# Performance work log

Measured on AMD Instinct MI355X. Metric: run time of the kernel, lower is better.

The kernel has to match this reference:

```python
import jax, jax.numpy as jnp
import numpy as np

B, C, H, W = 8, 512, 56, 56
CI = C // 2  # inter_channels
EPS = 1e-5   # BatchNorm eps


def setup_inputs() -> dict:
    key = jax.random.key(0)
    ks = jax.random.split(key, 11)
    s = 0.02
    return {
        "x": jax.random.normal(ks[0], (B, C, H, W), jnp.float32),
        "theta_w": jax.random.normal(ks[1], (CI, C), jnp.float32) * s,
        "theta_b": jnp.zeros((CI,), jnp.float32),
        "phi_w": jax.random.normal(ks[2], (CI, C), jnp.float32) * s,
        "phi_b": jnp.zeros((CI,), jnp.float32),
        "g_w": jax.random.normal(ks[3], (CI, C), jnp.float32) * s,
        "g_b": jnp.zeros((CI,), jnp.float32),
        "w_w": jax.random.normal(ks[4], (C, CI), jnp.float32) * s,
        "w_b": jnp.zeros((C,), jnp.float32),
        "bn_gamma": jax.random.normal(ks[5], (C,), jnp.float32) * 0.1,
        "bn_beta": jax.random.normal(ks[6], (C,), jnp.float32) * 0.1,
    }


def reference(x, theta_w, theta_b, phi_w, phi_b, g_w, g_b, w_w, w_b, bn_gamma, bn_beta):
    b, c, h, w = x.shape
    n = h * w

    def proj(wt, bi):  # 1x1 conv -> [b, out, n]
        return (jnp.einsum('bchw,oc->bohw', x, wt) + bi[None, :, None, None]).reshape(b, -1, n)

    theta_x = proj(theta_w, theta_b).transpose(0, 2, 1)  # [b, n, ci]
    phi_x = proj(phi_w, phi_b)                           # [b, ci, n]
    g_x = proj(g_w, g_b).transpose(0, 2, 1)             # [b, n, ci]

    f = jnp.einsum('bnc,bcm->bnm', theta_x, phi_x)       # [b, n, n] unscaled scores
    f_div_c = jax.nn.softmax(f, axis=-1)
    y = jnp.einsum('bnm,bmc->bnc', f_div_c, g_x)         # [b, n, ci]
    y = y.transpose(0, 2, 1).reshape(b, -1, h, w)        # [b, ci, h, w]

    w_y = jnp.einsum('bchw,oc->bohw', y, w_w) + w_b[None, :, None, None]
    # BatchNorm2d (training mode, batch statistics over B,H,W per channel)
    mean = w_y.mean(axis=(0, 2, 3))
    var = w_y.var(axis=(0, 2, 3))
    w_y = (w_y - mean[None, :, None, None]) * jax.lax.rsqrt(var[None, :, None, None] + EPS)
    w_y = w_y * bn_gamma[None, :, None, None] + bn_beta[None, :, None, None]
    return w_y + x
```

## Files before the change

### kernel.cpp

```cpp
#include <hip/hip_runtime.h>
#include <hip/hip_bf16.h>


typedef unsigned short u16;
typedef unsigned int u32;
typedef __attribute__((ext_vector_type(8))) short short8;
typedef __attribute__((ext_vector_type(4))) float floatx4;

#define B_   8
#define C_   512
#define CI_  256
#define N_   3136
#define BN_  25088

__device__ __forceinline__ u16 f2b(float f) {
    return __builtin_bit_cast(u16, __float2bfloat16(f));
}
__device__ __forceinline__ float b2f(u16 u) {
    return __bfloat162float(__builtin_bit_cast(__hip_bfloat16, u));
}
__device__ __forceinline__ floatx4 mfma16(short8 a, short8 b, floatx4 c) {
    return __builtin_amdgcn_mfma_f32_16x16x32_bf16(a, b, c, 0, 0, 0);
}
__device__ __forceinline__ void gload_lds16(const u16* g, u16* l) {
    __builtin_amdgcn_global_load_lds(
        (const __attribute__((address_space(1))) u32*)g,
        (__attribute__((address_space(3))) u32*)l, 16, 0, 0);
}

__global__ void detect_dtype(const u32* __restrict__ xw, int* __restrict__ flag)
{
    __shared__ int cnt;
    if (threadIdx.x == 0) cnt = 0;
    __syncthreads();
    int c = 0;
    for (int i = 0; i < 16; ++i) {
        u32 w = xw[threadIdx.x * 16 + i];
        u32 e = (w >> 7) & 0xFF;
        c += (e >= 118 && e <= 130) ? 1 : 0;
    }
    atomicAdd(&cnt, c);
    __syncthreads();
    if (threadIdx.x == 0) *flag = (2 * cnt > 4096) ? 1 : 0;
}

__global__ __launch_bounds__(256) void convert_params(
    const void* tw, const void* tb, const void* pw, const void* pb,
    const void* gw, const void* gbi, const void* ww, const void* wb,
    const void* gamma, const void* beta,
    u16* __restrict__ dst, const int* __restrict__ flag)
{
    const void* srcs[10] = {tw, tb, pw, pb, gw, gbi, ww, wb, gamma, beta};
    const int ns[10] = {131072, 256, 131072, 256, 131072, 256, 131072, 512, 512, 512};
    int seg = blockIdx.y;
    int off = 0;
    for (int s = 0; s < 10; ++s) { if (s == seg) break; off += ns[s]; }
    const void* src = srcs[seg];
    int n = ns[seg];
    int i0 = (blockIdx.x * 256 + threadIdx.x) * 8;
    if (i0 >= n) return;
    const int fl = *flag;
    u16* d = dst + off;
    for (int k = 0; k < 8; ++k) {
        int i = i0 + k;
        if (i < n)
            d[i] = fl ? ((const u16*)src)[i] : f2b(((const float*)src)[i]);
    }
}

__global__ __launch_bounds__(256) void transpose_x(
    const void* __restrict__ in, u16* __restrict__ out,
    const int* __restrict__ flag)
{
    __shared__ u16 tile[64][68];
    const int fl = *flag;
    const int t = threadIdx.x;
    const long base = (long)blockIdx.z * (long)C_ * (long)N_;
    const int c0 = blockIdx.x * 64, r0 = blockIdx.y * 64;
    const int lr = t >> 3;
    const int lc = (t & 7) * 8;
#pragma unroll
    for (int j = 0; j < 2; ++j) {
        int rr = lr + 32 * j;
        long eoff = base + (long)(r0 + rr) * N_ + c0 + lc;
        u16 v[8] __attribute__((aligned(16)));
        if (fl) {
            const u16* pi = (const u16*)in + eoff;
            *(uint64_t*)&v[0] = *(const uint64_t*)pi;
            *(uint64_t*)&v[4] = *(const uint64_t*)(pi + 4);
        } else {
            const float* pi = (const float*)in + eoff;
            floatx4 a = *(const floatx4*)pi;
            floatx4 b4 = *(const floatx4*)(pi + 4);
#pragma unroll
            for (int k = 0; k < 4; ++k) { v[k] = f2b(a[k]); v[4 + k] = f2b(b4[k]); }
        }
        *(uint64_t*)&tile[rr][lc] = *(const uint64_t*)&v[0];
        *(uint64_t*)&tile[rr][lc + 4] = *(const uint64_t*)&v[4];
    }
    __syncthreads();
#pragma unroll
    for (int j = 0; j < 2; ++j) {
        int oc = lr + 32 * j;
        int ob = (t & 7) * 8;
        u16 vals[8] __attribute__((aligned(16)));
#pragma unroll
        for (int k = 0; k < 8; ++k) vals[k] = tile[ob + k][oc];
        u16* po = out + (long)blockIdx.z * N_ * C_ + (long)(c0 + oc) * C_ + r0 + ob;
        *(uint64_t*)po = *(const uint64_t*)vals;
        *(uint64_t*)(po + 4) = *(const uint64_t*)(vals + 4);
    }
}

__global__ __launch_bounds__(256) void transpose64(
    const u16* __restrict__ in, u16* __restrict__ out, int R, int Cc)
{
    __shared__ u16 tile[64][68];
    const int t = threadIdx.x;
    const long base = (long)blockIdx.z * (long)R * (long)Cc;
    const int c0 = blockIdx.x * 64, r0 = blockIdx.y * 64;
    const int lr = t >> 3;
    const int lc = (t & 7) * 8;
#pragma unroll
    for (int j = 0; j < 2; ++j) {
        int rr = lr + 32 * j;
        const u16* pi = in + base + (long)(r0 + rr) * Cc + c0 + lc;
        *(uint64_t*)&tile[rr][lc] = *(const uint64_t*)pi;
        *(uint64_t*)&tile[rr][lc + 4] = *(const uint64_t*)(pi + 4);
    }
    __syncthreads();
#pragma unroll
    for (int j = 0; j < 2; ++j) {
        int oc = lr + 32 * j;
        int ob = (t & 7) * 8;
        u16 vals[8] __attribute__((aligned(16)));
#pragma unroll
        for (int k = 0; k < 8; ++k) vals[k] = tile[ob + k][oc];
        u16* po = out + base + (long)(c0 + oc) * R + r0 + ob;
        *(uint64_t*)po = *(const uint64_t*)vals;
        *(uint64_t*)(po + 4) = *(const uint64_t*)(vals + 4);
    }
}

template<int K>
__global__ __launch_bounds__(256, 3) void gemm128(
    const u16* __restrict__ A,
    const u16* __restrict__ BtBase,
    const u16* __restrict__ biasBase,
    u16* __restrict__ OutBase,
    int ncols, long bstride, long ostride)
{
    __shared__ __attribute__((aligned(16))) u16 Asf[2][8][64][8];
    __shared__ __attribute__((aligned(16))) u16 Bsf[2][8][64][8];

    const int t = threadIdx.x;
    const int wave = t >> 6, lane = t & 63;
    const int q = lane >> 4, lx = lane & 15;
    const int m0 = blockIdx.x * 128;
    const int n0 = blockIdx.y * 128;
    const u16* Bt = BtBase + (long)blockIdx.z * bstride;
    const u16* bias = biasBase + (long)blockIdx.z * bstride;
    u16* Out = OutBase + (long)blockIdx.z * ostride;

    floatx4 zero4 = {0.f, 0.f, 0.f, 0.f};
    floatx4 acc[4][4];
#pragma unroll
    for (int i = 0; i < 4; ++i)
#pragma unroll
        for (int j = 0; j < 4; ++j) acc[i][j] = zero4;

    auto stage = [&](int buf, int k0) {
#pragma unroll
        for (int i = 0; i < 2; ++i) {
            int rg = wave * 2 + i;
            gload_lds16(A + (long)(m0 + rg * 16 + lx) * K + k0 + q * 8,
                        &Asf[buf][rg][0][0]);
            gload_lds16(Bt + (long)(n0 + rg * 16 + lx) * K + k0 + q * 8,
                        &Bsf[buf][rg][0][0]);
        }
    };

    stage(0, 0);
    const int rg0 = (wave >> 1) * 4, cg0 = (wave & 1) * 4;
    const int NS = K / 32;
    for (int s = 0; s < NS; ++s) {
        const int buf = s & 1;
        __syncthreads();
        if (s + 1 < NS) stage(buf ^ 1, (s + 1) * 32);
        short8 af[4], bfr[4];
#pragma unroll
        for (int i = 0; i < 4; ++i)
            af[i] = *(const short8*)&Asf[buf][rg0 + i][lane][0];
#pragma unroll
        for (int j = 0; j < 4; ++j)
            bfr[j] = *(const short8*)&Bsf[buf][cg0 + j][lane][0];
#pragma unroll
        for (int i = 0; i < 4; ++i)
#pragma unroll
            for (int j = 0; j < 4; ++j)
                acc[i][j] = mfma16(af[i], bfr[j], acc[i][j]);
    }

    const int wr = (wave >> 1) * 64, wc = (wave & 1) * 64;
#pragma unroll
    for (int j = 0; j < 4; ++j) {
        int col = n0 + wc + j * 16 + lx;
        float bv = b2f(bias[col]);
#pragma unroll
        for (int i = 0; i < 4; ++i) {
#pragma unroll
            for (int r = 0; r < 4; ++r) {
                int row = m0 + wr + i * 16 + q * 4 + r;
                Out[(long)row * ncols + col] = f2b(acc[i][j][r] + bv);
            }
        }
    }
}

__global__ __launch_bounds__(256, 2) void attn(
    const u16* __restrict__ theta,
    const u16* __restrict__ phi,
    const u16* __restrict__ gT,
    u16* __restrict__ ypart,
    float* __restrict__ lpart)
{
    __shared__ __attribute__((aligned(16))) u16 psf[2][8][2][64][8];
    __shared__ __attribute__((aligned(16))) u16 gsf[2][16][64][8];
    __shared__ __attribute__((aligned(16))) u16 Ps[4][32][40];

    const int t = threadIdx.x;
    const int wave = t >> 6, lane = t & 63;
    const int q = lane >> 4, lx = lane & 15;
    const int b = blockIdx.y;
    const int z = blockIdx.z;
    const int n0w = blockIdx.x * 128 + wave * 32;
    const bool valid = n0w < N_;
    const u16* thb = theta + (long)b * N_ * CI_;
    const u16* phb = phi + (long)b * N_ * CI_;
    const u16* gb = gT + (long)b * CI_ * N_;

    short8 tf[2][8];
#pragma unroll
    for (int h = 0; h < 2; ++h) {
        int trow = n0w + h * 16 + lx;
        if (trow >= N_) trow = N_ - 1;
#pragma unroll
        for (int kk = 0; kk < 8; ++kk)
            tf[h][kk] = *(const short8*)(thb + (long)trow * CI_ + kk * 32 + q * 8);
    }

    floatx4 zero4 = {0.f, 0.f, 0.f, 0.f};
    floatx4 yacc[2][16];
#pragma unroll
    for (int h = 0; h < 2; ++h)
#pragma unroll
        for (int i = 0; i < 16; ++i) yacc[h][i] = zero4;
    floatx4 lacc[2] = {zero4, zero4};
    const short8 ones = {0x3F80, 0x3F80, 0x3F80, 0x3F80,
                         0x3F80, 0x3F80, 0x3F80, 0x3F80};

    const int mbeg = z * (N_ / 2);

    auto stage = [&](int buf, int m0) {
#pragma unroll
        for (int i = 0; i < 2; ++i) {
            int kc = wave * 2 + i;
#pragma unroll
            for (int h = 0; h < 2; ++h)
                gload_lds16(phb + (long)(m0 + h * 16 + lx) * CI_ + kc * 32 + q * 8,
                            &psf[buf][kc][h][0][0]);
        }
#pragma unroll
        for (int j4 = 0; j4 < 4; ++j4) {
            int ct = wave * 4 + j4;
            gload_lds16(gb + (long)(ct * 16 + lx) * N_ + m0 + q * 8,
                        &gsf[buf][ct][0][0]);
        }
    };

    stage(0, mbeg);
    const int NSTEP = (N_ / 2) / 32;
    for (int s = 0; s < NSTEP; ++s) {
        const int buf = s & 1;
        __syncthreads();
        if (s + 1 < NSTEP) stage(buf ^ 1, mbeg + (s + 1) * 32);

        floatx4 sacc[2][2];
        sacc[0][0] = zero4; sacc[0][1] = zero4;
        sacc[1][0] = zero4; sacc[1][1] = zero4;
#pragma unroll
        for (int half = 0; half < 2; ++half) {
            short8 pb0[4], pb1[4];
#pragma unroll
            for (int u = 0; u < 4; ++u) {
                int kk = half * 4 + u;
                pb0[u] = *(const short8*)&psf[buf][kk][0][lane][0];
                pb1[u] = *(const short8*)&psf[buf][kk][1][lane][0];
            }
#pragma unroll
            for (int u = 0; u < 4; ++u) {
                int kk = half * 4 + u;
                sacc[0][0] = mfma16(tf[0][kk], pb0[u], sacc[0][0]);
                sacc[1][0] = mfma16(tf[1][kk], pb0[u], sacc[1][0]);
                sacc[0][1] = mfma16(tf[0][kk], pb1[u], sacc[0][1]);
                sacc[1][1] = mfma16(tf[1][kk], pb1[u], sacc[1][1]);
            }
        }

#pragma unroll
        for (int h = 0; h < 2; ++h)
#pragma unroll
            for (int mh = 0; mh < 2; ++mh)
#pragma unroll
                for (int r = 0; r < 4; ++r) {
                    float e = __expf(fminf(sacc[h][mh][r], 60.f));
                    Ps[wave][h * 16 + q * 4 + r][mh * 16 + lx] = f2b(e);
                }
        __builtin_amdgcn_wave_barrier();
        short8 pA0 = *(const short8*)&Ps[wave][lx][q * 8];
        short8 pA1 = *(const short8*)&Ps[wave][16 + lx][q * 8];
        __builtin_amdgcn_wave_barrier();

#pragma unroll
        for (int ct = 0; ct < 16; ++ct) {
            short8 gf = *(const short8*)&gsf[buf][ct][lane][0];
            yacc[0][ct] = mfma16(pA0, gf, yacc[0][ct]);
            yacc[1][ct] = mfma16(pA1, gf, yacc[1][ct]);
        }
        lacc[0] = mfma16(pA0, ones, lacc[0]);
        lacc[1] = mfma16(pA1, ones, lacc[1]);
    }

    if (valid) {
        u16* yb = ypart + (long)z * B_ * N_ * CI_ + (long)b * N_ * CI_;
#pragma unroll
        for (int h = 0; h < 2; ++h)
#pragma unroll
            for (int ct = 0; ct < 16; ++ct)
#pragma unroll
                for (int r = 0; r < 4; ++r)
                    yb[(long)(n0w + h * 16 + q * 4 + r) * CI_ + ct * 16 + lx] =
                        f2b(yacc[h][ct][r]);
        if (lx == 0) {
#pragma unroll
            for (int h = 0; h < 2; ++h)
#pragma unroll
                for (int r = 0; r < 4; ++r)
                    lpart[(long)z * BN_ + (long)b * N_ + n0w + h * 16 + q * 4 + r] =
                        lacc[h][r];
        }
    }
}

__global__ __launch_bounds__(256) void attn_combine(
    const u16* __restrict__ ypart, const float* __restrict__ lpart,
    u16* __restrict__ y)
{
    long tt = (long)blockIdx.x * 256 + threadIdx.x;
    long row = tt >> 5;
    int cb = (int)(tt & 31) * 8;
    float l = lpart[row] + lpart[BN_ + row];
    float rl = 1.0f / l;
    const u16* p0 = ypart + row * CI_ + cb;
    const u16* p1 = p0 + (long)B_ * N_ * CI_;
    short8 v0 = *(const short8*)p0;
    short8 v1 = *(const short8*)p1;
    u16 ov[8] __attribute__((aligned(16)));
#pragma unroll
    for (int j = 0; j < 8; ++j)
        ov[j] = f2b((b2f(((const u16*)&v0)[j]) + b2f(((const u16*)&v1)[j])) * rl);
    *(short8*)(y + row * CI_ + cb) = *(const short8*)ov;
}

__global__ void zero_stats(float* stats) {
    stats[threadIdx.x] = 0.f;
    stats[threadIdx.x + 256] = 0.f;
    stats[threadIdx.x + 512] = 0.f;
    stats[threadIdx.x + 768] = 0.f;
}

__global__ __launch_bounds__(256) void bn_stats(
    const u16* __restrict__ wy, float* __restrict__ stats)
{
    const int t = threadIdx.x;
    const long row0 = (long)blockIdx.x * 256;
    float s0 = 0.f, s1 = 0.f, q0 = 0.f, q1 = 0.f;
    for (int r = 0; r < 256; ++r) {
        const u16* p = wy + (row0 + r) * C_;
        float a = b2f(p[t]), b = b2f(p[t + 256]);
        s0 += a; q0 += a * a;
        s1 += b; q1 += b * b;
    }
    atomicAdd(&stats[t], s0);
    atomicAdd(&stats[t + 256], s1);
    atomicAdd(&stats[C_ + t], q0);
    atomicAdd(&stats[C_ + t + 256], q1);
}

__global__ __launch_bounds__(256) void bn_apply(
    const u16* __restrict__ wy, const void* __restrict__ xv,
    const u16* __restrict__ gamma, const u16* __restrict__ beta,
    const float* __restrict__ stats, void* __restrict__ outv,
    const int* __restrict__ flag)
{
    __shared__ float tile[64][65];
    const int fl = *flag;
    const int t = threadIdx.x;
    const int nb0 = blockIdx.x * 64;
    const int c0 = blockIdx.y * 64;
    const int b = blockIdx.z;
#pragma unroll
    for (int j = 0; j < 4; ++j) {
        int row = (t >> 4) + 16 * j;
        int col = (t & 15) * 4;
        const u16* p = wy + ((long)b * N_ + nb0 + row) * C_ + c0 + col;
        u16 lv[4] __attribute__((aligned(8)));
        *(uint64_t*)lv = *(const uint64_t*)p;
#pragma unroll
        for (int k = 0; k < 4; ++k) tile[row][col + k] = b2f(lv[k]);
    }
    __syncthreads();
    const float inv = 1.0f / (float)BN_;
#pragma unroll
    for (int it = 0; it < 8; ++it) {
        int oc = (t >> 5) + 8 * it;
        int on = (t & 31) * 2;
        int c = c0 + oc;
        float mean = stats[c] * inv;
        float var = stats[C_ + c] * inv - mean * mean;
        float rstd = rsqrtf(var + 1e-5f);
        float sc = b2f(gamma[c]) * rstd;
        float sh = b2f(beta[c]) - mean * sc;
        long base = ((long)b * C_ + c) * N_ + nb0 + on;
        float v0 = tile[on][oc] * sc + sh;
        float v1 = tile[on + 1][oc] * sc + sh;
        if (fl) {
            v0 += b2f(((const u16*)xv)[base]);
            v1 += b2f(((const u16*)xv)[base + 1]);
            ((u16*)outv)[base] = f2b(v0);
            ((u16*)outv)[base + 1] = f2b(v1);
        } else {
            v0 += ((const float*)xv)[base];
            v1 += ((const float*)xv)[base + 1];
            ((float*)outv)[base] = v0;
            ((float*)outv)[base + 1] = v1;
        }
    }
}

extern "C" void kernel_launch(void* const* d_in, const int* in_sizes, int n_in,
                              void* d_out, int out_size, void* d_ws, size_t ws_size,
                              hipStream_t stream)
{
    (void)in_sizes; (void)n_in; (void)out_size; (void)ws_size;

    const size_t S = 12845056;
    char* base = (char*)d_ws;
    u16*   xT    = (u16*)(base);
    u16*   gT    = (u16*)(base);
    u16*   y     = (u16*)(base + S);
    u16*   th    = (u16*)(base + 2 * S);
    u16*   wy    = (u16*)(base + 2 * S);
    u16*   gn    = (u16*)(base + 4 * S);
    float* lpart = (float*)(base + 5 * S);
    float* stats = (float*)(base + 5 * S + (size_t)2 * BN_ * 4);
    u16*   cw    = (u16*)(base + 5 * S + (size_t)2 * BN_ * 4 + 4096);
    int*   flag  = (int*)(base + 5 * S + (size_t)2 * BN_ * 4 + 4096 + 1055744);

    u16* ctw = cw;               u16* ctb = cw + 131072;
    u16* cpw = ctb + 256;        u16* cpb = cpw + 131072;
    u16* cgw = cpb + 256;        u16* cgb = cgw + 131072;
    u16* cww = cgb + 256;        u16* cwb = cww + 131072;
    u16* cga = cwb + 512;        u16* cbe = cga + 512;
    (void)cpw; (void)cpb; (void)cgw; (void)cgb;

    u16* ypart = (u16*)d_out;

    detect_dtype<<<1, 256, 0, stream>>>((const u32*)d_in[0], flag);
    convert_params<<<dim3(64, 10), 256, 0, stream>>>(
        d_in[1], d_in[2], d_in[3], d_in[4], d_in[5], d_in[6], d_in[7],
        d_in[8], d_in[9], d_in[10], cw, flag);

    transpose_x<<<dim3(N_ / 64, C_ / 64, B_), 256, 0, stream>>>(d_in[0], xT, flag);

    gemm128<C_><<<dim3(BN_ / 128, CI_ / 128, 3), 256, 0, stream>>>(
        xT, ctw, ctb, th, CI_, 131328L, (long)(S / 2));

    transpose64<<<dim3(CI_ / 64, N_ / 64, B_), 256, 0, stream>>>(gn, gT, N_, CI_);

    attn<<<dim3(25, B_, 2), 256, 0, stream>>>(th, th + S / 2, gT, ypart, lpart);

    attn_combine<<<dim3((BN_ * 32) / 256), 256, 0, stream>>>(ypart, lpart, y);

    gemm128<CI_><<<dim3(BN_ / 128, C_ / 128, 1), 256, 0, stream>>>(
        y, cww, cwb, wy, C_, 0L, 0L);

    zero_stats<<<1, 256, 0, stream>>>(stats);
    bn_stats<<<BN_ / 256, 256, 0, stream>>>(wy, stats);

    bn_apply<<<dim3(N_ / 64, C_ / 64, B_), 256, 0, stream>>>(
        wy, d_in[0], cga, cbe, stats, d_out, flag);
}
```

Before: 382.8 us.

## Split attention key range four ways and trim small-kernel launches

Result: no change. 387.1 us (+1.1%).

```diff
diff --git a/kernel.cpp b/kernel.cpp
--- a/kernel.cpp
+++ b/kernel.cpp
@@ -28,7 +28,8 @@
         (__attribute__((address_space(3))) u32*)l, 16, 0, 0);
 }
 
-__global__ void detect_dtype(const u32* __restrict__ xw, int* __restrict__ flag)
+__global__ void detect_dtype(const u32* __restrict__ xw, int* __restrict__ flag,
+                             float* __restrict__ stats)
 {
     __shared__ int cnt;
     if (threadIdx.x == 0) cnt = 0;
@@ -40,6 +41,10 @@
         c += (e >= 118 && e <= 130) ? 1 : 0;
     }
     atomicAdd(&cnt, c);
+    stats[threadIdx.x] = 0.f;
+    stats[threadIdx.x + 256] = 0.f;
+    stats[threadIdx.x + 512] = 0.f;
+    stats[threadIdx.x + 768] = 0.f;
     __syncthreads();
     if (threadIdx.x == 0) *flag = (2 * cnt > 4096) ? 1 : 0;
 }
@@ -221,7 +226,8 @@
     const u16* __restrict__ theta,
     const u16* __restrict__ phi,
     const u16* __restrict__ gT,
-    u16* __restrict__ ypart,
+    u16* __restrict__ yp0, u16* __restrict__ yp1,
+    u16* __restrict__ yp2, u16* __restrict__ yp3,
     float* __restrict__ lpart)
 {
     __shared__ __attribute__((aligned(16))) u16 psf[2][8][2][64][8];
@@ -259,7 +265,8 @@
     const short8 ones = {0x3F80, 0x3F80, 0x3F80, 0x3F80,
                          0x3F80, 0x3F80, 0x3F80, 0x3F80};
 
-    const int mbeg = z * (N_ / 2);
+    const int mbeg = z * 800;
+    const int mend = (z == 3) ? N_ : mbeg + 800;
 
     auto stage = [&](int buf, int m0) {
 #pragma unroll
@@ -279,7 +286,7 @@
     };
 
     stage(0, mbeg);
-    const int NSTEP = (N_ / 2) / 32;
+    const int NSTEP = (mend - mbeg) / 32;
     for (int s = 0; s < NSTEP; ++s) {
         const int buf = s & 1;
         __syncthreads();
@@ -289,22 +296,13 @@
         sacc[0][0] = zero4; sacc[0][1] = zero4;
         sacc[1][0] = zero4; sacc[1][1] = zero4;
 #pragma unroll
-        for (int half = 0; half < 2; ++half) {
-            short8 pb0[4], pb1[4];
-#pragma unroll
-            for (int u = 0; u < 4; ++u) {
-                int kk = half * 4 + u;
-                pb0[u] = *(const short8*)&psf[buf][kk][0][lane][0];
-                pb1[u] = *(const short8*)&psf[buf][kk][1][lane][0];
-            }
-#pragma unroll
-            for (int u = 0; u < 4; ++u) {
-                int kk = half * 4 + u;
-                sacc[0][0] = mfma16(tf[0][kk], pb0[u], sacc[0][0]);
-                sacc[1][0] = mfma16(tf[1][kk], pb0[u], sacc[1][0]);
-                sacc[0][1] = mfma16(tf[0][kk], pb1[u], sacc[0][1]);
-                sacc[1][1] = mfma16(tf[1][kk], pb1[u], sacc[1][1]);
-            }
+        for (int kk = 0; kk < 8; ++kk) {
+            short8 bf0 = *(const short8*)&psf[buf][kk][0][lane][0];
+            short8 bf1 = *(const short8*)&psf[buf][kk][1][lane][0];
+            sacc[0][0] = mfma16(tf[0][kk], bf0, sacc[0][0]);
+            sacc[1][0] = mfma16(tf[1][kk], bf0, sacc[1][0]);
+            sacc[0][1] = mfma16(tf[0][kk], bf1, sacc[0][1]);
+            sacc[1][1] = mfma16(tf[1][kk], bf1, sacc[1][1]);
         }
 
 #pragma unroll
@@ -316,13 +314,22 @@
                     float e = __expf(fminf(sacc[h][mh][r], 60.f));
                     Ps[wave][h * 16 + q * 4 + r][mh * 16 + lx] = f2b(e);
                 }
+        short8 gpre[4];
+#pragma unroll
+        for (int j = 0; j < 4; ++j)
+            gpre[j] = *(const short8*)&gsf[buf][j][lane][0];
         __builtin_amdgcn_wave_barrier();
         short8 pA0 = *(const short8*)&Ps[wave][lx][q * 8];
         short8 pA1 = *(const short8*)&Ps[wave][16 + lx][q * 8];
         __builtin_amdgcn_wave_barrier();
 
 #pragma unroll
-        for (int ct = 0; ct < 16; ++ct) {
+        for (int j = 0; j < 4; ++j) {
+            yacc[0][j] = mfma16(pA0, gpre[j], yacc[0][j]);
+            yacc[1][j] = mfma16(pA1, gpre[j], yacc[1][j]);
+        }
+#pragma unroll
+        for (int ct = 4; ct < 16; ++ct) {
             short8 gf = *(const short8*)&gsf[buf][ct][lane][0];
             yacc[0][ct] = mfma16(pA0, gf, yacc[0][ct]);
             yacc[1][ct] = mfma16(pA1, gf, yacc[1][ct]);
@@ -332,7 +339,8 @@
     }
 
     if (valid) {
-        u16* yb = ypart + (long)z * B_ * N_ * CI_ + (long)b * N_ * CI_;
+        u16* ypz = (z == 0) ? yp0 : (z == 1) ? yp1 : (z == 2) ? yp2 : yp3;
+        u16* yb = ypz + (long)b * N_ * CI_;
 #pragma unroll
         for (int h = 0; h < 2; ++h)
 #pragma unroll
@@ -353,39 +361,36 @@
 }
 
 __global__ __launch_bounds__(256) void attn_combine(
-    const u16* __restrict__ ypart, const float* __restrict__ lpart,
-    u16* __restrict__ y)
+    const u16* __restrict__ yp0, const u16* __restrict__ yp1,
+    const u16* __restrict__ yp2, const u16* __restrict__ yp3,
+    const float* __restrict__ lpart, u16* __restrict__ y)
 {
     long tt = (long)blockIdx.x * 256 + threadIdx.x;
     long row = tt >> 5;
     int cb = (int)(tt & 31) * 8;
-    float l = lpart[row] + lpart[BN_ + row];
+    float l = lpart[row] + lpart[BN_ + row] + lpart[2 * BN_ + row]
+            + lpart[3 * BN_ + row];
     float rl = 1.0f / l;
-    const u16* p0 = ypart + row * CI_ + cb;
-    const u16* p1 = p0 + (long)B_ * N_ * CI_;
-    short8 v0 = *(const short8*)p0;
-    short8 v1 = *(const short8*)p1;
+    long off = row * CI_ + cb;
+    short8 v0 = *(const short8*)(yp0 + off);
+    short8 v1 = *(const short8*)(yp1 + off);
+    short8 v2 = *(const short8*)(yp2 + off);
+    short8 v3 = *(const short8*)(yp3 + off);
     u16 ov[8] __attribute__((aligned(16)));
 #pragma unroll
     for (int j = 0; j < 8; ++j)
-        ov[j] = f2b((b2f(((const u16*)&v0)[j]) + b2f(((const u16*)&v1)[j])) * rl);
-    *(short8*)(y + row * CI_ + cb) = *(const short8*)ov;
-}
-
-__global__ void zero_stats(float* stats) {
-    stats[threadIdx.x] = 0.f;
-    stats[threadIdx.x + 256] = 0.f;
-    stats[threadIdx.x + 512] = 0.f;
-    stats[threadIdx.x + 768] = 0.f;
+        ov[j] = f2b((b2f(((const u16*)&v0)[j]) + b2f(((const u16*)&v1)[j]) +
+                     b2f(((const u16*)&v2)[j]) + b2f(((const u16*)&v3)[j])) * rl);
+    *(short8*)(y + off) = *(const short8*)ov;
 }
 
 __global__ __launch_bounds__(256) void bn_stats(
     const u16* __restrict__ wy, float* __restrict__ stats)
 {
     const int t = threadIdx.x;
-    const long row0 = (long)blockIdx.x * 256;
+    const long row0 = (long)blockIdx.x * 32;
     float s0 = 0.f, s1 = 0.f, q0 = 0.f, q1 = 0.f;
-    for (int r = 0; r < 256; ++r) {
+    for (int r = 0; r < 32; ++r) {
         const u16* p = wy + (row0 + r) * C_;
         float a = b2f(p[t]), b = b2f(p[t + 256]);
         s0 += a; q0 += a * a;
@@ -455,6 +460,7 @@
     (void)in_sizes; (void)n_in; (void)out_size; (void)ws_size;
 
     const size_t S = 12845056;
+    const size_t SE = S / 2;
     char* base = (char*)d_ws;
     u16*   xT    = (u16*)(base);
     u16*   gT    = (u16*)(base);
@@ -463,20 +469,20 @@
     u16*   wy    = (u16*)(base + 2 * S);
     u16*   gn    = (u16*)(base + 4 * S);
     float* lpart = (float*)(base + 5 * S);
-    float* stats = (float*)(base + 5 * S + (size_t)2 * BN_ * 4);
-    u16*   cw    = (u16*)(base + 5 * S + (size_t)2 * BN_ * 4 + 4096);
-    int*   flag  = (int*)(base + 5 * S + (size_t)2 * BN_ * 4 + 4096 + 1055744);
+    float* stats = (float*)(base + 5 * S + (size_t)4 * BN_ * 4);
+    u16*   cw    = (u16*)(base + 5 * S + (size_t)4 * BN_ * 4 + 4096);
+    int*   flag  = (int*)(base + 5 * S + (size_t)4 * BN_ * 4 + 4096 + 1055744);
 
     u16* ctw = cw;               u16* ctb = cw + 131072;
-    u16* cpw = ctb + 256;        u16* cpb = cpw + 131072;
-    u16* cgw = cpb + 256;        u16* cgb = cgw + 131072;
-    u16* cww = cgb + 256;        u16* cwb = cww + 131072;
+    u16* cww = ctb + 256 + 2 * 131328;  u16* cwb = cww + 131072;
     u16* cga = cwb + 512;        u16* cbe = cga + 512;
-    (void)cpw; (void)cpb; (void)cgw; (void)cgb;
-
-    u16* ypart = (u16*)d_out;
-
-    detect_dtype<<<1, 256, 0, stream>>>((const u32*)d_in[0], flag);
+
+    u16* yp0 = (u16*)d_out;
+    u16* yp1 = (u16*)d_out + SE;
+    u16* yp2 = y;
+    u16* yp3 = gn;
+
+    detect_dtype<<<1, 256, 0, stream>>>((const u32*)d_in[0], flag, stats);
     convert_params<<<dim3(64, 10), 256, 0, stream>>>(
         d_in[1], d_in[2], d_in[3], d_in[4], d_in[5], d_in[6], d_in[7],
         d_in[8], d_in[9], d_in[10], cw, flag);
@@ -484,19 +490,20 @@
     transpose_x<<<dim3(N_ / 64, C_ / 64, B_), 256, 0, stream>>>(d_in[0], xT, flag);
 
     gemm128<C_><<<dim3(BN_ / 128, CI_ / 128, 3), 256, 0, stream>>>(
-        xT, ctw, ctb, th, CI_, 131328L, (long)(S / 2));
+        xT, ctw, ctb, th, CI_, 131328L, (long)SE);
 
     transpose64<<<dim3(CI_ / 64, N_ / 64, B_), 256, 0, stream>>>(gn, gT, N_, CI_);
 
-    attn<<<dim3(25, B_, 2), 256, 0, stream>>>(th, th + S / 2, gT, ypart, lpart);
-
-    attn_combine<<<dim3((BN_ * 32) / 256), 256, 0, stream>>>(ypart, lpart, y);
+    attn<<<dim3(25, B_, 4), 256, 0, stream>>>(
+        th, th + SE, gT, yp0, yp1, yp2, yp3, lpart);
+
+    attn_combine<<<dim3((BN_ * 32) / 256), 256, 0, stream>>>(
+        yp0, yp1, yp2, yp3, lpart, y);
 
     gemm128<CI_><<<dim3(BN_ / 128, C_ / 128, 1), 256, 0, stream>>>(
         y, cww, cwb, wy, C_, 0L, 0L);
 
-    zero_stats<<<1, 256, 0, stream>>>(stats);
-    bn_stats<<<BN_ / 256, 256, 0, stream>>>(wy, stats);
+    bn_stats<<<BN_ / 32, 256, 0, stream>>>(wy, stats);
 
     bn_apply<<<dim3(N_ / 64, C_ / 64, B_), 256, 0, stream>>>(
         wy, d_in[0], cga, cbe, stats, d_out, flag);
```
